# Kernel optimization log

Hardware: AMD Instinct MI355X
Metric: run time of the kernel (lower is better)

The kernel has to match this reference:

```python
import jax, jax.numpy as jnp
import numpy as np

D_MODEL = 1152
NUM_HEADS = 16
HEAD_DIM = D_MODEL // NUM_HEADS
B, N, M = 8, 4096, 300


def setup_inputs() -> dict:
    key = jax.random.key(0)
    ks = jax.random.split(key, 10)
    s = 0.02
    x = jax.random.normal(ks[0], (B, N, D_MODEL), dtype=jnp.float32)
    cond = jax.random.normal(ks[1], (B, M, D_MODEL), dtype=jnp.float32)
    # per-sample valid conditioning lengths in [1, M]
    mask = jax.random.randint(ks[2], (B,), 1, M + 1, dtype=jnp.int32)
    wq = jax.random.normal(ks[3], (D_MODEL, D_MODEL), dtype=jnp.float32) * s
    bq = jnp.zeros((D_MODEL,), dtype=jnp.float32)
    wkv = jax.random.normal(ks[4], (D_MODEL, 2 * D_MODEL), dtype=jnp.float32) * s
    bkv = jnp.zeros((2 * D_MODEL,), dtype=jnp.float32)
    wp = jax.random.normal(ks[5], (D_MODEL, D_MODEL), dtype=jnp.float32) * s
    bp = jnp.zeros((D_MODEL,), dtype=jnp.float32)
    return {"x": x, "cond": cond, "mask": mask, "wq": wq, "bq": bq,
            "wkv": wkv, "bkv": bkv, "wp": wp, "bp": bp}


def reference(x, cond, mask, wq, bq, wkv, bkv, wp, bp):
    b, n, c = x.shape
    m = cond.shape[1]
    # projections
    q = (x @ wq + bq).reshape(b, n, NUM_HEADS, HEAD_DIM)
    kv = (cond @ wkv + bkv).reshape(b, m, 2, NUM_HEADS, HEAD_DIM)
    k, v = kv[:, :, 0], kv[:, :, 1]
    scale = 1.0 / jnp.sqrt(jnp.asarray(HEAD_DIM, dtype=x.dtype))
    # [b, h, n, m] attention scores
    scores = jnp.einsum("bnhd,bmhd->bhnm", q, k) * scale
    # key positions j < mask[i] are valid (matches torch bool attn_mask)
    valid = (jnp.arange(m)[None, :] < mask[:, None])  # [b, m]
    bias = jnp.where(valid, 0.0, -1e9).astype(scores.dtype)[:, None, None, :]
    attn = jax.nn.softmax(scores + bias, axis=-1)
    out = jnp.einsum("bhnm,bmhd->bnhd", attn, v).reshape(b, n, c)
    return out @ wp + bp
```

## Files before the change

### kernel.cpp

```cpp
#include <hip/hip_runtime.h>
#include <cstdint>

typedef unsigned short u16;
typedef __attribute__((ext_vector_type(8))) short short8;
typedef __attribute__((ext_vector_type(4))) float floatx4;

__device__ __forceinline__ u16 f2bf(float f) {
    unsigned u = __float_as_uint(f);
    u += 0x7FFFu + ((u >> 16) & 1u);
    return (u16)(u >> 16);
}

__device__ __forceinline__ void async16(const void* g, void* l) {
    __builtin_amdgcn_global_load_lds(
        (const __attribute__((address_space(1))) unsigned*)g,
        (__attribute__((address_space(3))) unsigned*)l, 16, 0, 0);
}

__global__ void cast_bf16_kernel(const float* __restrict__ in, u16* __restrict__ out, long n8) {
    long i = (long)blockIdx.x * 256 + threadIdx.x;
    if (i >= n8) return;
    const float4* p = (const float4*)in;
    float4 a = p[i * 2], b = p[i * 2 + 1];
    uint4 o;
    o.x = f2bf(a.x) | ((unsigned)f2bf(a.y) << 16);
    o.y = f2bf(a.z) | ((unsigned)f2bf(a.w) << 16);
    o.z = f2bf(b.x) | ((unsigned)f2bf(b.y) << 16);
    o.w = f2bf(b.z) | ((unsigned)f2bf(b.w) << 16);
    ((uint4*)out)[i] = o;
}

__global__ void transpose_cast(const float* __restrict__ W, u16* __restrict__ Wt, int K, int N) {
    __shared__ float tile[32][33];
    int bx = blockIdx.x * 32, by = blockIdx.y * 32;
    int tx = threadIdx.x, ty = threadIdx.y;
#pragma unroll
    for (int i = 0; i < 32; i += 8)
        tile[ty + i][tx] = W[(long)(by + ty + i) * N + bx + tx];
    __syncthreads();
#pragma unroll
    for (int i = 0; i < 32; i += 8)
        Wt[(long)(bx + ty + i) * K + by + tx] = f2bf(tile[tx][ty + i]);
}

template <int MODE>
__global__ __launch_bounds__(256)
void gemm_bt(const u16* __restrict__ A, const u16* __restrict__ Bt,
             const float* __restrict__ bias, float scale,
             u16* __restrict__ outA, u16* __restrict__ outB, float* __restrict__ outF,
             int M, int N, int K) {
    __shared__ u16 As[128 * 32];
    __shared__ u16 Bs[128 * 32];
    const int tid = threadIdx.x, lane = tid & 63, wave = tid >> 6;
    const int wm = wave >> 1, wn = wave & 1;
    const int quad = lane >> 4, cl = lane & 15;
    const long rowBase = (long)blockIdx.x * 128;
    const int colBase = blockIdx.y * 128;
    const int srow = lane >> 2;
    const int skc = (lane & 3) * 8;

    floatx4 acc[4][4];
#pragma unroll
    for (int i = 0; i < 4; i++)
#pragma unroll
        for (int j = 0; j < 4; j++) acc[i][j] = (floatx4){0.f, 0.f, 0.f, 0.f};

    for (int k0 = 0; k0 < K; k0 += 32) {
#pragma unroll
        for (int j = 0; j < 2; ++j) {
            int inst = wave * 2 + j;
            long r = rowBase + inst * 16 + srow;
            if (r > (long)M - 1) r = (long)M - 1;
            async16(A + r * K + k0 + skc, &As[inst * 512]);
        }
#pragma unroll
        for (int j = 0; j < 2; ++j) {
            int inst = wave * 2 + j;
            long r = colBase + inst * 16 + srow;
            async16(Bt + r * K + k0 + skc, &Bs[inst * 512]);
        }
        __syncthreads();
        short8 af[4], bf[4];
#pragma unroll
        for (int mi = 0; mi < 4; mi++)
            af[mi] = *(const short8*)&As[(wm * 64 + mi * 16 + cl) * 32 + quad * 8];
#pragma unroll
        for (int ni = 0; ni < 4; ni++)
            bf[ni] = *(const short8*)&Bs[(wn * 64 + ni * 16 + cl) * 32 + quad * 8];
#pragma unroll
        for (int mi = 0; mi < 4; mi++)
#pragma unroll
            for (int ni = 0; ni < 4; ni++)
                acc[mi][ni] = __builtin_amdgcn_mfma_f32_16x16x32_bf16(af[mi], bf[ni], acc[mi][ni], 0, 0, 0);
        __syncthreads();
    }

#pragma unroll
    for (int mi = 0; mi < 4; mi++) {
        long row0 = rowBase + wm * 64 + mi * 16 + quad * 4;
#pragma unroll
        for (int ni = 0; ni < 4; ni++) {
            int col = colBase + wn * 64 + ni * 16 + cl;
            float bv = bias[col];
#pragma unroll
            for (int r = 0; r < 4; r++) {
                long row = row0 + r;
                if (row < M) {
                    float v = (acc[mi][ni][r] + bv) * scale;
                    if (MODE == 0) {
                        outA[row * N + col] = f2bf(v);
                    } else if (MODE == 1) {
                        int bb = (int)(row / 300);
                        int mm = (int)(row - (long)bb * 300);
                        if (col < 1152) {
                            int hh = col / 72, dd = col - hh * 72;
                            outA[(((long)bb * 16 + hh) * 300 + mm) * 72 + dd] = f2bf(v);
                        } else {
                            int c2 = col - 1152;
                            int hh = c2 / 72, dd = c2 - hh * 72;
                            outB[(((long)bb * 16 + hh) * 72 + dd) * 304 + mm] = f2bf(v);
                        }
                    } else {
                        outF[row * (long)N + col] = v;
                    }
                }
            }
        }
    }
}

__global__ __launch_bounds__(256)
void attn_kernel(const u16* __restrict__ Q, const u16* __restrict__ K,
                 const u16* __restrict__ V, const int* __restrict__ mask,
                 u16* __restrict__ O) {
    __shared__ u16 Qs[64 * 104];
    __shared__ u16 Ks[96 * 104];
    __shared__ u16 Vs[80 * 104];
    __shared__ u16 Ps[64 * 104];

    const int tid = threadIdx.x, lane = tid & 63, wave = tid >> 6;
    const int quad = lane >> 4, cl = lane & 15;
    const int b = blockIdx.z, h = blockIdx.y, nt = blockIdx.x;
    int mb = mask[b];
    if (mb > 300) mb = 300;
    if (mb < 1) mb = 1;

    const long qbase = ((long)b * 4096 + nt * 64) * 1152 + h * 72;
    for (int idx = tid; idx < 768; idx += 256) {
        int r = idx / 12, c = idx - r * 12;
        uint4 v = {0, 0, 0, 0};
        if (c < 9) v = *(const uint4*)(Q + qbase + (long)r * 1152 + c * 8);
        *(uint4*)&Qs[r * 104 + c * 8] = v;
    }
    for (int idx = tid; idx < 288; idx += 256) {
        int m = idx / 3, c = idx - m * 3;
        *(uint4*)&Ks[m * 104 + 72 + c * 8] = (uint4){0, 0, 0, 0};
    }
    for (int idx = tid; idx < 104; idx += 256) {
        int dd = 72 + idx / 13, c = idx - (idx / 13) * 13;
        unsigned fill = (dd == 72) ? 0x3F803F80u : 0u;
        *(uint4*)&Vs[dd * 104 + c * 8] = (uint4){fill, fill, fill, fill};
    }

    floatx4 oacc[5];
#pragma unroll
    for (int i = 0; i < 5; i++) oacc[i] = (floatx4){0.f, 0.f, 0.f, 0.f};

    const int bh = b * 16 + h;
    const u16* kb = K + (long)bh * 300 * 72;
    const u16* vb = V + (long)bh * 72 * 304;

    const int nch = (mb + 95) / 96;
    for (int ch = 0; ch < nch; ++ch) {
        const int base = ch * 96;
        __syncthreads();
        for (int idx = tid; idx < 864; idx += 256) {
            int m = idx / 9, c = idx - m * 9;
            int mg = base + m;
            uint4 v = {0, 0, 0, 0};
            if (mg < 300) v = *(const uint4*)(kb + (long)mg * 72 + c * 8);
            *(uint4*)&Ks[m * 104 + c * 8] = v;
        }
        for (int idx = tid; idx < 864; idx += 256) {
            int dd = idx / 12, c = idx - dd * 12;
            int off = base + c * 8;
            uint4 v = {0, 0, 0, 0};
            if (off < 304) v = *(const uint4*)(vb + (long)dd * 304 + off);
            *(uint4*)&Vs[dd * 104 + c * 8] = v;
        }
        __syncthreads();

        floatx4 sacc[6];
#pragma unroll
        for (int t = 0; t < 6; t++) sacc[t] = (floatx4){0.f, 0.f, 0.f, 0.f};
#pragma unroll
        for (int kk = 0; kk < 3; ++kk) {
            short8 af = *(const short8*)&Qs[(wave * 16 + cl) * 104 + kk * 32 + quad * 8];
#pragma unroll
            for (int t = 0; t < 6; t++) {
                short8 bfr = *(const short8*)&Ks[(t * 16 + cl) * 104 + kk * 32 + quad * 8];
                sacc[t] = __builtin_amdgcn_mfma_f32_16x16x32_bf16(af, bfr, sacc[t], 0, 0, 0);
            }
        }

#pragma unroll
        for (int r = 0; r < 4; r++) {
            int prow = (wave * 16 + quad * 4 + r) * 104;
#pragma unroll
            for (int t = 0; t < 6; t++) {
                int col = base + t * 16 + cl;
                float p = (col < mb) ? __expf(sacc[t][r]) : 0.f;
                Ps[prow + t * 16 + cl] = f2bf(p);
            }
        }
        __syncthreads();

#pragma unroll
        for (int kk = 0; kk < 3; ++kk) {
            short8 pf = *(const short8*)&Ps[(wave * 16 + cl) * 104 + kk * 32 + quad * 8];
#pragma unroll
            for (int dt = 0; dt < 5; dt++) {
                short8 vf = *(const short8*)&Vs[(dt * 16 + cl) * 104 + kk * 32 + quad * 8];
                oacc[dt] = __builtin_amdgcn_mfma_f32_16x16x32_bf16(pf, vf, oacc[dt], 0, 0, 0);
            }
        }
    }

#pragma unroll
    for (int r = 0; r < 4; r++) {
        float l = __shfl(oacc[4][r], (lane & 48) + 8);
        float inv = 1.0f / l;
        int row = wave * 16 + quad * 4 + r;
#pragma unroll
        for (int dt = 0; dt < 5; dt++) {
            int dd = dt * 16 + cl;
            if (dd < 72) O[qbase + (long)row * 1152 + dd] = f2bf(oacc[dt][r] * inv);
        }
    }
}

extern "C" void kernel_launch(void* const* d_in, const int* in_sizes, int n_in,
                              void* d_out, int out_size, void* d_ws, size_t ws_size,
                              hipStream_t stream) {
    const float* x    = (const float*)d_in[0];
    const float* cond = (const float*)d_in[1];
    const int*   mask = (const int*)d_in[2];
    const float* wq   = (const float*)d_in[3];
    const float* bq   = (const float*)d_in[4];
    const float* wkv  = (const float*)d_in[5];
    const float* bkv  = (const float*)d_in[6];
    const float* wp   = (const float*)d_in[7];
    const float* bp   = (const float*)d_in[8];

    char* ws = (char*)d_ws;
    u16* xb    = (u16*)(ws);
    u16* condb = (u16*)(ws + 75497472ll);
    u16* wqT   = (u16*)(ws + 81027072ll);
    u16* wkvT  = (u16*)(ws + 83681280ll);
    u16* wpT   = (u16*)(ws + 88989696ll);
    u16* qbuf  = (u16*)(ws + 91643904ll);
    u16* kbuf  = (u16*)(ws + 167141376ll);
    u16* vbuf  = (u16*)(ws + 172670976ll);
    if (ws_size < 178200576ull) return;

    cast_bf16_kernel<<<18432, 256, 0, stream>>>(x, xb, 4718592ll);
    cast_bf16_kernel<<<1350, 256, 0, stream>>>(cond, condb, 345600ll);
    transpose_cast<<<dim3(36, 36), dim3(32, 8), 0, stream>>>(wq, wqT, 1152, 1152);
    transpose_cast<<<dim3(72, 36), dim3(32, 8), 0, stream>>>(wkv, wkvT, 1152, 2304);
    transpose_cast<<<dim3(36, 36), dim3(32, 8), 0, stream>>>(wp, wpT, 1152, 1152);

    gemm_bt<0><<<dim3(256, 9), 256, 0, stream>>>(xb, wqT, bq, 0.11785113019775793f,
                                                 qbuf, nullptr, nullptr, 32768, 1152, 1152);
    gemm_bt<1><<<dim3(19, 18), 256, 0, stream>>>(condb, wkvT, bkv, 1.0f,
                                                 kbuf, vbuf, nullptr, 2400, 2304, 1152);
    attn_kernel<<<dim3(64, 16, 8), 256, 0, stream>>>(qbuf, kbuf, vbuf, mask, xb);
    gemm_bt<2><<<dim3(256, 9), 256, 0, stream>>>(xb, wpT, bp, 1.0f,
                                                 nullptr, nullptr, (float*)d_out, 32768, 1152, 1152);
}
```

Baseline: 747.2 us.

## Restructure attention: 128-key chunks, padded swizzled K/V layout, async LDS loads

The KV projection now writes K padded to 384 keys and V in 128-key chunks with an XOR-swizzled column layout, so the attention kernel can fetch each chunk with global_load_lds async copies instead of bounds-checked register staging. Q fragments are held in registers rather than LDS. The P tile reuses the K buffer, which shrinks shared memory, and launch bounds ask for 4 blocks per CU. Workspace is reordered so wqT and wpT alias the K/V region, which requires a zero fill of the K/V buffers and moving the wp transpose after attention.

```diff
diff --git a/kernel.cpp b/kernel.cpp
--- a/kernel.cpp
+++ b/kernel.cpp
@@ -28,6 +28,11 @@
     o.z = f2bf(b.x) | ((unsigned)f2bf(b.y) << 16);
     o.w = f2bf(b.z) | ((unsigned)f2bf(b.w) << 16);
     ((uint4*)out)[i] = o;
+}
+
+__global__ void fill_zero(uint4* __restrict__ p, int n) {
+    int i = blockIdx.x * 256 + threadIdx.x;
+    if (i < n) p[i] = (uint4){0u, 0u, 0u, 0u};
 }
 
 __global__ void transpose_cast(const float* __restrict__ W, u16* __restrict__ Wt, int K, int N) {
@@ -114,11 +119,13 @@
                         int mm = (int)(row - (long)bb * 300);
                         if (col < 1152) {
                             int hh = col / 72, dd = col - hh * 72;
-                            outA[(((long)bb * 16 + hh) * 300 + mm) * 72 + dd] = f2bf(v);
+                            outA[((long)(bb * 16 + hh) * 384 + mm) * 72 + dd] = f2bf(v);
                         } else {
                             int c2 = col - 1152;
                             int hh = c2 / 72, dd = c2 - hh * 72;
-                            outB[(((long)bb * 16 + hh) * 72 + dd) * 304 + mm] = f2bf(v);
+                            int ch = mm >> 7, mc = mm & 127;
+                            int g = (mc >> 3) ^ (dd & 7);
+                            outB[(((long)(bb * 16 + hh) * 3 + ch) * 72 + dd) * 128 + g * 8 + (mc & 7)] = f2bf(v);
                         }
                     } else {
                         outF[row * (long)N + col] = v;
@@ -129,14 +136,13 @@
     }
 }
 
-__global__ __launch_bounds__(256)
+__global__ __launch_bounds__(256, 4)
 void attn_kernel(const u16* __restrict__ Q, const u16* __restrict__ K,
                  const u16* __restrict__ V, const int* __restrict__ mask,
                  u16* __restrict__ O) {
-    __shared__ u16 Qs[64 * 104];
-    __shared__ u16 Ks[96 * 104];
-    __shared__ u16 Vs[80 * 104];
-    __shared__ u16 Ps[64 * 104];
+    __shared__ __align__(16) u16 smem[(18432 + 20480) / 2];
+    u16* Ks = smem;
+    u16* Vs = smem + 9216;
 
     const int tid = threadIdx.x, lane = tid & 63, wave = tid >> 6;
     const int quad = lane >> 4, cl = lane & 15;
@@ -144,83 +150,76 @@
     int mb = mask[b];
     if (mb > 300) mb = 300;
     if (mb < 1) mb = 1;
+    const int bh = b * 16 + h;
 
     const long qbase = ((long)b * 4096 + nt * 64) * 1152 + h * 72;
-    for (int idx = tid; idx < 768; idx += 256) {
-        int r = idx / 12, c = idx - r * 12;
-        uint4 v = {0, 0, 0, 0};
-        if (c < 9) v = *(const uint4*)(Q + qbase + (long)r * 1152 + c * 8);
-        *(uint4*)&Qs[r * 104 + c * 8] = v;
-    }
-    for (int idx = tid; idx < 288; idx += 256) {
-        int m = idx / 3, c = idx - m * 3;
-        *(uint4*)&Ks[m * 104 + 72 + c * 8] = (uint4){0, 0, 0, 0};
-    }
-    for (int idx = tid; idx < 104; idx += 256) {
-        int dd = 72 + idx / 13, c = idx - (idx / 13) * 13;
-        unsigned fill = (dd == 72) ? 0x3F803F80u : 0u;
-        *(uint4*)&Vs[dd * 104 + c * 8] = (uint4){fill, fill, fill, fill};
+
+    const u16* qrow = Q + qbase + (long)(wave * 16 + cl) * 1152;
+    short8 zero8 = {0, 0, 0, 0, 0, 0, 0, 0};
+    short8 aq[3];
+    aq[0] = *(const short8*)(qrow + quad * 8);
+    aq[1] = *(const short8*)(qrow + 32 + quad * 8);
+    aq[2] = (quad == 0) ? *(const short8*)(qrow + 64) : zero8;
+
+    if (tid < 16) {
+        unsigned fill = 0x3F803F80u;
+        *(uint4*)&Vs[72 * 128 + tid * 8] = (uint4){fill, fill, fill, fill};
     }
 
     floatx4 oacc[5];
 #pragma unroll
     for (int i = 0; i < 5; i++) oacc[i] = (floatx4){0.f, 0.f, 0.f, 0.f};
 
-    const int bh = b * 16 + h;
-    const u16* kb = K + (long)bh * 300 * 72;
-    const u16* vb = V + (long)bh * 72 * 304;
-
-    const int nch = (mb + 95) / 96;
+    const u16* kb = K + (long)bh * 384 * 72;
+    const u16* vb = V + (long)bh * 3 * 9216;
+
+    const int nch = (mb + 127) >> 7;
     for (int ch = 0; ch < nch; ++ch) {
-        const int base = ch * 96;
-        __syncthreads();
-        for (int idx = tid; idx < 864; idx += 256) {
-            int m = idx / 9, c = idx - m * 9;
-            int mg = base + m;
-            uint4 v = {0, 0, 0, 0};
-            if (mg < 300) v = *(const uint4*)(kb + (long)mg * 72 + c * 8);
-            *(uint4*)&Ks[m * 104 + c * 8] = v;
-        }
-        for (int idx = tid; idx < 864; idx += 256) {
-            int dd = idx / 12, c = idx - dd * 12;
-            int off = base + c * 8;
-            uint4 v = {0, 0, 0, 0};
-            if (off < 304) v = *(const uint4*)(vb + (long)dd * 304 + off);
-            *(uint4*)&Vs[dd * 104 + c * 8] = v;
-        }
-        __syncthreads();
-
-        floatx4 sacc[6];
-#pragma unroll
-        for (int t = 0; t < 6; t++) sacc[t] = (floatx4){0.f, 0.f, 0.f, 0.f};
+        const int base = ch << 7;
+        __syncthreads();
+
+        const u16* ksrc = kb + (long)base * 72;
+        for (int i = wave; i < 18; i += 4)
+            async16(ksrc + i * 512 + lane * 8, Ks + i * 512);
+        const u16* vsrc = vb + (long)ch * 9216;
+        for (int i = wave; i < 18; i += 4)
+            async16(vsrc + i * 512 + lane * 8, Vs + i * 512);
+        __syncthreads();
+
+        floatx4 sacc[8];
+#pragma unroll
+        for (int t = 0; t < 8; t++) sacc[t] = (floatx4){0.f, 0.f, 0.f, 0.f};
 #pragma unroll
         for (int kk = 0; kk < 3; ++kk) {
-            short8 af = *(const short8*)&Qs[(wave * 16 + cl) * 104 + kk * 32 + quad * 8];
-#pragma unroll
-            for (int t = 0; t < 6; t++) {
-                short8 bfr = *(const short8*)&Ks[(t * 16 + cl) * 104 + kk * 32 + quad * 8];
-                sacc[t] = __builtin_amdgcn_mfma_f32_16x16x32_bf16(af, bfr, sacc[t], 0, 0, 0);
-            }
-        }
-
-#pragma unroll
-        for (int r = 0; r < 4; r++) {
-            int prow = (wave * 16 + quad * 4 + r) * 104;
-#pragma unroll
-            for (int t = 0; t < 6; t++) {
+#pragma unroll
+            for (int t = 0; t < 8; ++t) {
+                short8 bfr = *(const short8*)&Ks[(t * 16 + cl) * 72 + kk * 32 + quad * 8];
+                sacc[t] = __builtin_amdgcn_mfma_f32_16x16x32_bf16(aq[kk], bfr, sacc[t], 0, 0, 0);
+            }
+        }
+        __syncthreads();
+
+#pragma unroll
+        for (int r = 0; r < 4; ++r) {
+            int prow = (wave * 16 + quad * 4 + r) * 136;
+#pragma unroll
+            for (int t = 0; t < 8; ++t) {
                 int col = base + t * 16 + cl;
                 float p = (col < mb) ? __expf(sacc[t][r]) : 0.f;
-                Ps[prow + t * 16 + cl] = f2bf(p);
-            }
-        }
-        __syncthreads();
-
-#pragma unroll
-        for (int kk = 0; kk < 3; ++kk) {
-            short8 pf = *(const short8*)&Ps[(wave * 16 + cl) * 104 + kk * 32 + quad * 8];
-#pragma unroll
-            for (int dt = 0; dt < 5; dt++) {
-                short8 vf = *(const short8*)&Vs[(dt * 16 + cl) * 104 + kk * 32 + quad * 8];
+                unsigned pb = f2bf(p);
+                unsigned ob = __shfl_xor(pb, 1);
+                if (!(lane & 1))
+                    *(unsigned*)&Ks[prow + t * 16 + cl] = pb | (ob << 16);
+            }
+        }
+
+#pragma unroll
+        for (int kk = 0; kk < 4; ++kk) {
+            short8 pf = *(const short8*)&Ks[(wave * 16 + cl) * 136 + kk * 32 + quad * 8];
+#pragma unroll
+            for (int dt = 0; dt < 5; ++dt) {
+                int dd = dt * 16 + cl;
+                short8 vf = *(const short8*)&Vs[dd * 128 + (((kk * 4 + quad) ^ (dd & 7)) << 3)];
                 oacc[dt] = __builtin_amdgcn_mfma_f32_16x16x32_bf16(pf, vf, oacc[dt], 0, 0, 0);
             }
         }
@@ -255,25 +254,26 @@
     char* ws = (char*)d_ws;
     u16* xb    = (u16*)(ws);
     u16* condb = (u16*)(ws + 75497472ll);
-    u16* wqT   = (u16*)(ws + 81027072ll);
-    u16* wkvT  = (u16*)(ws + 83681280ll);
-    u16* wpT   = (u16*)(ws + 88989696ll);
-    u16* qbuf  = (u16*)(ws + 91643904ll);
-    u16* kbuf  = (u16*)(ws + 167141376ll);
-    u16* vbuf  = (u16*)(ws + 172670976ll);
-    if (ws_size < 178200576ull) return;
+    u16* wkvT  = (u16*)(ws + 81027072ll);
+    u16* qbuf  = (u16*)(ws + 86335488ll);
+    u16* kbuf  = (u16*)(ws + 161832960ll);
+    u16* vbuf  = (u16*)(ws + 168910848ll);
+    u16* wqT   = (u16*)(ws + 161832960ll);
+    u16* wpT   = (u16*)(ws + 161832960ll);
+    if (ws_size < 175988736ull) return;
 
     cast_bf16_kernel<<<18432, 256, 0, stream>>>(x, xb, 4718592ll);
     cast_bf16_kernel<<<1350, 256, 0, stream>>>(cond, condb, 345600ll);
     transpose_cast<<<dim3(36, 36), dim3(32, 8), 0, stream>>>(wq, wqT, 1152, 1152);
     transpose_cast<<<dim3(72, 36), dim3(32, 8), 0, stream>>>(wkv, wkvT, 1152, 2304);
-    transpose_cast<<<dim3(36, 36), dim3(32, 8), 0, stream>>>(wp, wpT, 1152, 1152);
 
     gemm_bt<0><<<dim3(256, 9), 256, 0, stream>>>(xb, wqT, bq, 0.11785113019775793f,
                                                  qbuf, nullptr, nullptr, 32768, 1152, 1152);
+    fill_zero<<<3456, 256, 0, stream>>>((uint4*)kbuf, 884736);
     gemm_bt<1><<<dim3(19, 18), 256, 0, stream>>>(condb, wkvT, bkv, 1.0f,
                                                  kbuf, vbuf, nullptr, 2400, 2304, 1152);
     attn_kernel<<<dim3(64, 16, 8), 256, 0, stream>>>(qbuf, kbuf, vbuf, mask, xb);
+    transpose_cast<<<dim3(36, 36), dim3(32, 8), 0, stream>>>(wp, wpT, 1152, 1152);
     gemm_bt<2><<<dim3(256, 9), 256, 0, stream>>>(xb, wpT, bp, 1.0f,
                                                  nullptr, nullptr, (float*)d_out, 32768, 1152, 1152);
 }
```

Result: faster. 689.8 us (-7.7%).
